# Kernel tuning notes

Measured on AMD Instinct MI355X. Metric: run time of the kernel, lower is better.

The kernel has to match this reference:

```python
import jax, jax.numpy as jnp
import numpy as np

A, B, S, AD, H, NH = 8, 32768, 128, 16, 64, 4
D = H // NH  # attend_dim = 16
MAX_ACTION = 1.0


def setup_inputs() -> dict:
    key = jax.random.key(0)
    ks = jax.random.split(key, 16)
    sc = 0.05
    return {
        'states': jax.random.normal(ks[0], (A, B, S), jnp.float32),
        'actions': jax.random.normal(ks[1], (A, B, AD), jnp.float32),
        'Ws': jax.random.normal(ks[2], (S, H), jnp.float32) * sc,
        'bs': jnp.zeros((H,), jnp.float32),
        'We': jax.random.normal(ks[3], (S + AD, H), jnp.float32) * sc,
        'be': jnp.zeros((H,), jnp.float32),
        'Wk': jax.random.normal(ks[4], (NH, H, D), jnp.float32) * sc,
        'Wsel': jax.random.normal(ks[5], (NH, H, D), jnp.float32) * sc,
        'Wv': jax.random.normal(ks[6], (NH, H, D), jnp.float32) * sc,
        'bv': jnp.zeros((NH, D), jnp.float32),
        'W1': jax.random.normal(ks[7], (2 * H, H), jnp.float32) * sc,
        'b1': jnp.zeros((H,), jnp.float32),
        'W2': jax.random.normal(ks[8], (H, 1), jnp.float32) * sc,
        'b2': jnp.zeros((1,), jnp.float32),
    }


def reference(states, actions, Ws, bs, We, be, Wk, Wsel, Wv, bv, W1, b1, W2, b2):
    # per-agent encoders (shared params, as in the torch module)
    s_enc = jax.nn.relu(jnp.einsum('abs,sh->abh', states, Ws) + bs)          # [A,B,H]
    sa = jnp.concatenate([states, actions / MAX_ACTION], axis=-1)            # [A,B,S+AD]
    sa_enc = jax.nn.relu(jnp.einsum('abi,ih->abh', sa, We) + be)             # [A,B,H]

    # per-head keys / values / selectors (n = head axis)
    keys = jnp.einsum('abh,nhd->nabd', sa_enc, Wk)                           # [NH,A,B,D]
    vals = jax.nn.relu(jnp.einsum('abh,nhd->nabd', sa_enc, Wv) + bv[:, None, None, :])
    sel = jnp.einsum('abh,nhd->nabd', s_enc, Wsel)                           # [NH,A,B,D]

    # exclude-self attention over agents == masked softmax over agent axis j
    logits = jnp.einsum('nibd,njbd->nibj', sel, keys) / jnp.sqrt(jnp.float32(D))
    self_mask = jnp.eye(A, dtype=bool)                                       # [A(i),A(j)]
    logits = jnp.where(self_mask[None, :, None, :], -1e9, logits)
    w = jax.nn.softmax(logits, axis=-1)                                      # [NH,A,B,A]
    other = jnp.einsum('nibj,njbd->nibd', w, vals)                           # [NH,A,B,D]
    other_cat = jnp.transpose(other, (1, 2, 0, 3)).reshape(A, B, NH * D)     # [A,B,H]

    critic_in = jnp.concatenate([sa_enc, other_cat], axis=-1)                # [A,B,2H]
    h = jax.nn.relu(jnp.einsum('abi,ih->abh', critic_in, W1) + b1)
    q = jnp.einsum('abh,ho->abo', h, W2) + b2                                # [A,B,1]
    return q
```

## Files before the change

### kernel.cpp

```cpp
#include <hip/hip_runtime.h>
#include <hip/hip_bf16.h>

#define A_N 8
#define B_N 32768
#define S_N 128
#define AD_N 16

typedef __attribute__((ext_vector_type(8))) short short8;
typedef __attribute__((ext_vector_type(4))) float floatx4;

#define MFMA16(a, b, c) __builtin_amdgcn_mfma_f32_16x16x32_bf16(a, b, c, 0, 0, 0)

__device__ __forceinline__ short f2bf(float f) {
    __hip_bfloat16 h = __float2bfloat16(f);
    return *reinterpret_cast<short*>(&h);
}
__device__ __forceinline__ float bf2f(short s) {
    return __uint_as_float(((unsigned)(unsigned short)s) << 16);
}
__device__ __forceinline__ void pk2(short8& r, int i, float a, float b) {
    __hip_bfloat162 p = __float22bfloat162_rn(make_float2(a, b));
    short2 s = *reinterpret_cast<short2*>(&p);
    r[i] = s.x; r[i + 1] = s.y;
}
__device__ __forceinline__ short8 cvt8(float4 x0, float4 x1) {
    short8 r;
    pk2(r, 0, x0.x, x0.y); pk2(r, 2, x0.z, x0.w);
    pk2(r, 4, x1.x, x1.y); pk2(r, 6, x1.z, x1.w);
    return r;
}
__device__ __forceinline__ void wait_lgkm() {
    asm volatile("s_waitcnt lgkmcnt(0)" ::: "memory");
}

#define OFF_Ws 10752
#define OFF_Wk 19456
#define OFF_Wsel 24064
#define OFF_Wv 28672
#define OFF_W1 33280
#define W_TOTAL 41984

__global__ void prep_weights(const float* __restrict__ Ws, const float* __restrict__ We,
                             const float* __restrict__ Wk, const float* __restrict__ Wsel,
                             const float* __restrict__ Wv, const float* __restrict__ W1,
                             short* __restrict__ w) {
    int idx = blockIdx.x * 256 + threadIdx.x;
    if (idx >= W_TOTAL) return;
    float v;
    if (idx < OFF_Ws)        { int n = idx / 168, k = idx % 168; v = (k < 144) ? We[k * 64 + n] : 0.f; }
    else if (idx < OFF_Wk)   { int i = idx - OFF_Ws;  int n = i / 136, k = i % 136; v = (k < 128) ? Ws[k * 64 + n] : 0.f; }
    else if (idx < OFF_Wsel) { int i = idx - OFF_Wk;  int n = i / 72,  k = i % 72;  v = (k < 64) ? Wk[(n >> 4) * 1024 + k * 16 + (n & 15)] : 0.f; }
    else if (idx < OFF_Wv)   { int i = idx - OFF_Wsel;int n = i / 72,  k = i % 72;  v = (k < 64) ? Wsel[(n >> 4) * 1024 + k * 16 + (n & 15)] : 0.f; }
    else if (idx < OFF_W1)   { int i = idx - OFF_Wv;  int n = i / 72,  k = i % 72;  v = (k < 64) ? Wv[(n >> 4) * 1024 + k * 16 + (n & 15)] : 0.f; }
    else                     { int i = idx - OFF_W1;  int n = i / 136, k = i % 136; v = (k < 128) ? W1[k * 64 + n] : 0.f; }
    w[idx] = f2bf(v);
}

#define ST 72
#define OFF_Eb 41984
#define OFF_Tb 51200
#define OFF_Kb 60416
#define OFF_Vb 69632
#define SMEM_TOT 78848

#define TILES 4

__global__ __launch_bounds__(512, 2)
void attention_critic_mfma(
    const float* __restrict__ states, const float* __restrict__ actions,
    const float* __restrict__ bs, const float* __restrict__ be,
    const float* __restrict__ bv, const float* __restrict__ b1,
    const float* __restrict__ W2, const float* __restrict__ b2,
    const short* __restrict__ wts, float* __restrict__ out)
{
    __shared__ __align__(16) short smem[SMEM_TOT];
    short* lWe   = smem;
    short* lWs   = smem + OFF_Ws;
    short* lWk   = smem + OFF_Wk;
    short* lWsel = smem + OFF_Wsel;
    short* lWv   = smem + OFF_Wv;
    short* lW1   = smem + OFF_W1;
    short* Eb    = smem + OFF_Eb;
    short* Tb    = smem + OFF_Tb;
    short* Kb    = smem + OFF_Kb;
    short* Vb    = smem + OFF_Vb;

    const int tid  = threadIdx.x;
    const int wv   = tid >> 6;
    const int lane = tid & 63;
    const int lq   = lane >> 4;
    const int ln   = lane & 15;
    const int rA   = wv * 16 + ln;
    const int bbase = blockIdx.x * (TILES * 16);

    for (int c = wv; c < 82; c += 8) {
        const unsigned int* g = reinterpret_cast<const unsigned int*>(wts + c * 512) + lane * 4;
        __builtin_amdgcn_global_load_lds(g, reinterpret_cast<unsigned int*>(smem + c * 512), 16, 0, 0);
    }

    const int aA  = ln & 7;
    const int blA = ln >> 3;
    const float* srow = states  + ((long)aA * B_N + bbase + wv * 2 + blA) * S_N;
    const float* arow = actions + ((long)aA * B_N + bbase + wv * 2 + blA) * AD_N;

    float4 ps[8]; float4 pa[2];
    #pragma unroll
    for (int s = 0; s < 4; ++s) {
        ps[2 * s]     = *reinterpret_cast<const float4*>(srow + s * 32 + lq * 8);
        ps[2 * s + 1] = *reinterpret_cast<const float4*>(srow + s * 32 + lq * 8 + 4);
    }
    if (lq < 2) {
        pa[0] = *reinterpret_cast<const float4*>(arow + lq * 8);
        pa[1] = *reinterpret_cast<const float4*>(arow + lq * 8 + 4);
    }
    __syncthreads();

    const floatx4 z = {0.f, 0.f, 0.f, 0.f};

    #pragma unroll 1
    for (int t = 0; t < TILES; ++t) {
        const int b0 = bbase + t * 16;

        floatx4 accE[4] = {z, z, z, z};
        floatx4 accS[4] = {z, z, z, z};
        #pragma unroll
        for (int s = 0; s < 4; ++s) {
            const int kk = s * 32 + lq * 8;
            short8 af = cvt8(ps[2 * s], ps[2 * s + 1]);
            #pragma unroll
            for (int nt = 0; nt < 4; ++nt) {
                short8 bE = *reinterpret_cast<const short8*>(lWe + (nt * 16 + ln) * 168 + kk);
                short8 bS = *reinterpret_cast<const short8*>(lWs + (nt * 16 + ln) * 136 + kk);
                accE[nt] = MFMA16(af, bE, accE[nt]);
                accS[nt] = MFMA16(af, bS, accS[nt]);
            }
        }
        {
            const int kk = 128 + lq * 8;
            short8 af = {0, 0, 0, 0, 0, 0, 0, 0};
            if (lq < 2) af = cvt8(pa[0], pa[1]);
            #pragma unroll
            for (int nt = 0; nt < 4; ++nt) {
                short8 bE = *reinterpret_cast<const short8*>(lWe + (nt * 16 + ln) * 168 + kk);
                accE[nt] = MFMA16(af, bE, accE[nt]);
            }
        }

        if (t + 1 < TILES) {
            srow += 16 * S_N; arow += 16 * AD_N;
            #pragma unroll
            for (int s = 0; s < 4; ++s) {
                ps[2 * s]     = *reinterpret_cast<const float4*>(srow + s * 32 + lq * 8);
                ps[2 * s + 1] = *reinterpret_cast<const float4*>(srow + s * 32 + lq * 8 + 4);
            }
            if (lq < 2) {
                pa[0] = *reinterpret_cast<const float4*>(arow + lq * 8);
                pa[1] = *reinterpret_cast<const float4*>(arow + lq * 8 + 4);
            }
        }

        #pragma unroll
        for (int nt = 0; nt < 4; ++nt) {
            const int col = nt * 16 + ln;
            const float bE = be[col], bS = bs[col];
            #pragma unroll
            for (int i = 0; i < 4; ++i) {
                const int row = wv * 16 + lq * 4 + i;
                Eb[row * ST + col] = f2bf(fmaxf(accE[nt][i] + bE, 0.f));
                Tb[row * ST + col] = f2bf(fmaxf(accS[nt][i] + bS, 0.f));
            }
        }
        wait_lgkm();

        floatx4 accSel[4] = {z, z, z, z};
        #pragma unroll
        for (int s = 0; s < 2; ++s) {
            short8 af = *reinterpret_cast<const short8*>(Tb + rA * ST + s * 32 + lq * 8);
            #pragma unroll
            for (int nt = 0; nt < 4; ++nt)
                accSel[nt] = MFMA16(af, *reinterpret_cast<const short8*>(lWsel + (nt * 16 + ln) * 72 + s * 32 + lq * 8), accSel[nt]);
        }
        #pragma unroll
        for (int nt = 0; nt < 4; ++nt)
            #pragma unroll
            for (int i = 0; i < 4; ++i)
                Tb[(wv * 16 + lq * 4 + i) * ST + nt * 16 + ln] = f2bf(accSel[nt][i]);

        floatx4 accK[4] = {z, z, z, z}, accV[4] = {z, z, z, z};
        #pragma unroll
        for (int s = 0; s < 2; ++s) {
            short8 af = *reinterpret_cast<const short8*>(Eb + rA * ST + s * 32 + lq * 8);
            #pragma unroll
            for (int nt = 0; nt < 4; ++nt) {
                accK[nt] = MFMA16(af, *reinterpret_cast<const short8*>(lWk + (nt * 16 + ln) * 72 + s * 32 + lq * 8), accK[nt]);
                accV[nt] = MFMA16(af, *reinterpret_cast<const short8*>(lWv + (nt * 16 + ln) * 72 + s * 32 + lq * 8), accV[nt]);
            }
        }
        #pragma unroll
        for (int nt = 0; nt < 4; ++nt) {
            const int col = nt * 16 + ln;
            const float bV = bv[col];
            #pragma unroll
            for (int i = 0; i < 4; ++i) {
                const int row = wv * 16 + lq * 4 + i;
                Kb[row * ST + col] = f2bf(accK[nt][i]);
                Vb[row * ST + col] = f2bf(fmaxf(accV[nt][i] + bV, 0.f));
            }
        }
        wait_lgkm();

        {
            const int r3 = lane >> 2;
            const int hn = lane & 3;
            const int a3 = r3 & 7;
            const int rowbase = wv * 16 + (r3 & 8);
            const int co = hn * 16;
            float selv[16];
            short8 s0 = *reinterpret_cast<const short8*>(Tb + (wv * 16 + r3) * ST + co);
            short8 s1 = *reinterpret_cast<const short8*>(Tb + (wv * 16 + r3) * ST + co + 8);
            #pragma unroll
            for (int d = 0; d < 8; ++d) { selv[d] = bf2f(s0[d]); selv[d + 8] = bf2f(s1[d]); }
            float lg[8];
            #pragma unroll
            for (int j = 0; j < 8; ++j) {
                const int rj = rowbase + j;
                short8 k0 = *reinterpret_cast<const short8*>(Kb + rj * ST + co);
                short8 k1 = *reinterpret_cast<const short8*>(Kb + rj * ST + co + 8);
                float acc = 0.f;
                #pragma unroll
                for (int d = 0; d < 8; ++d) acc += selv[d] * bf2f(k0[d]) + selv[d + 8] * bf2f(k1[d]);
                lg[j] = (j == a3) ? -1e9f : acc * 0.25f;
            }
            float m = lg[0];
            #pragma unroll
            for (int j = 1; j < 8; ++j) m = fmaxf(m, lg[j]);
            float e[8], ssum = 0.f;
            #pragma unroll
            for (int j = 0; j < 8; ++j) { e[j] = __expf(lg[j] - m); ssum += e[j]; }
            const float inv = 1.f / ssum;
            float oth[16];
            #pragma unroll
            for (int d = 0; d < 16; ++d) oth[d] = 0.f;
            #pragma unroll
            for (int j = 0; j < 8; ++j) {
                const float wj = e[j] * inv;
                const int rj = rowbase + j;
                short8 v0 = *reinterpret_cast<const short8*>(Vb + rj * ST + co);
                short8 v1 = *reinterpret_cast<const short8*>(Vb + rj * ST + co + 8);
                #pragma unroll
                for (int d = 0; d < 8; ++d) { oth[d] += wj * bf2f(v0[d]); oth[d + 8] += wj * bf2f(v1[d]); }
            }
            short8 o0, o1;
            #pragma unroll
            for (int d = 0; d < 8; ++d) { o0[d] = f2bf(oth[d]); o1[d] = f2bf(oth[d + 8]); }
            *reinterpret_cast<short8*>(Tb + (wv * 16 + r3) * ST + co)     = o0;
            *reinterpret_cast<short8*>(Tb + (wv * 16 + r3) * ST + co + 8) = o1;
        }
        wait_lgkm();

        floatx4 accH[4] = {z, z, z, z};
        #pragma unroll
        for (int s = 0; s < 4; ++s) {
            short8 af = (s < 2)
                ? *reinterpret_cast<const short8*>(Eb + rA * ST + s * 32 + lq * 8)
                : *reinterpret_cast<const short8*>(Tb + rA * ST + (s - 2) * 32 + lq * 8);
            #pragma unroll
            for (int nt = 0; nt < 4; ++nt)
                accH[nt] = MFMA16(af, *reinterpret_cast<const short8*>(lW1 + (nt * 16 + ln) * 136 + s * 32 + lq * 8), accH[nt]);
        }
        float p0 = 0.f, p1 = 0.f, p2 = 0.f, p3 = 0.f;
        #pragma unroll
        for (int nt = 0; nt < 4; ++nt) {
            const int col = nt * 16 + ln;
            const float w2v = W2[col], bb = b1[col];
            p0 += fmaxf(accH[nt][0] + bb, 0.f) * w2v;
            p1 += fmaxf(accH[nt][1] + bb, 0.f) * w2v;
            p2 += fmaxf(accH[nt][2] + bb, 0.f) * w2v;
            p3 += fmaxf(accH[nt][3] + bb, 0.f) * w2v;
        }
        #pragma unroll
        for (int mk = 1; mk < 16; mk <<= 1) {
            p0 += __shfl_xor(p0, mk, 64);
            p1 += __shfl_xor(p1, mk, 64);
            p2 += __shfl_xor(p2, mk, 64);
            p3 += __shfl_xor(p3, mk, 64);
        }
        if (ln == 0) {
            const float b2v = b2[0];
            float pr[4] = {p0, p1, p2, p3};
            #pragma unroll
            for (int i = 0; i < 4; ++i) {
                const int m = lq * 4 + i;
                out[(long)(m & 7) * B_N + b0 + wv * 2 + (m >> 3)] = pr[i] + b2v;
            }
        }
    }
}

extern "C" void kernel_launch(void* const* d_in, const int* in_sizes, int n_in,
                              void* d_out, int out_size, void* d_ws, size_t ws_size,
                              hipStream_t stream) {
    const float* states  = (const float*)d_in[0];
    const float* actions = (const float*)d_in[1];
    const float* Ws      = (const float*)d_in[2];
    const float* bs      = (const float*)d_in[3];
    const float* We      = (const float*)d_in[4];
    const float* be      = (const float*)d_in[5];
    const float* Wk      = (const float*)d_in[6];
    const float* Wsel    = (const float*)d_in[7];
    const float* Wv      = (const float*)d_in[8];
    const float* bv      = (const float*)d_in[9];
    const float* W1      = (const float*)d_in[10];
    const float* b1      = (const float*)d_in[11];
    const float* W2      = (const float*)d_in[12];
    const float* b2      = (const float*)d_in[13];
    short* wts = (short*)d_ws;
    float* out = (float*)d_out;

    prep_weights<<<(W_TOTAL + 255) / 256, 256, 0, stream>>>(Ws, We, Wk, Wsel, Wv, W1, wts);
    attention_critic_mfma<<<B_N / (TILES * 16), 512, 0, stream>>>(
        states, actions, bs, be, bv, b1, W2, b2, wts, out);
}
```

Measured before the change: 257.2 us.

## Keep intermediates in registers via transposed MFMA chaining and MFMA-based attention

Removes all shared-memory staging of activations. Each matmul's output fragment is chained directly as the next MFMA operand, using a channel permutation baked into the weights and transposed operand order. The per-agent attention logits and weighted sum now run as small MFMAs with shuffle-based softmax. Biases are folded into the encoder GEMM through a constant-one input column. Block size grows to 1024 threads with only weights in LDS, which trades register pressure and wasted zero-padded MFMA lanes for removing LDS traffic and barriers.

```diff
diff --git a/kernel.cpp b/kernel.cpp
--- a/kernel.cpp
+++ b/kernel.cpp
@@ -8,6 +8,7 @@
 
 typedef __attribute__((ext_vector_type(8))) short short8;
 typedef __attribute__((ext_vector_type(4))) float floatx4;
+typedef __attribute__((ext_vector_type(4))) int intx4;
 
 #define MFMA16(a, b, c) __builtin_amdgcn_mfma_f32_16x16x32_bf16(a, b, c, 0, 0, 0)
 
@@ -15,8 +16,13 @@
     __hip_bfloat16 h = __float2bfloat16(f);
     return *reinterpret_cast<short*>(&h);
 }
-__device__ __forceinline__ float bf2f(short s) {
-    return __uint_as_float(((unsigned)(unsigned short)s) << 16);
+__device__ __forceinline__ int pk(float a, float b) {
+    __hip_bfloat162 p = __float22bfloat162_rn(make_float2(a, b));
+    return *reinterpret_cast<int*>(&p);
+}
+__device__ __forceinline__ short8 mk8(int a, int b, int c, int d) {
+    intx4 v = {a, b, c, d};
+    return *reinterpret_cast<short8*>(&v);
 }
 __device__ __forceinline__ void pk2(short8& r, int i, float a, float b) {
     __hip_bfloat162 p = __float22bfloat162_rn(make_float2(a, b));
@@ -29,75 +35,86 @@
     pk2(r, 4, x1.x, x1.y); pk2(r, 6, x1.z, x1.w);
     return r;
 }
-__device__ __forceinline__ void wait_lgkm() {
-    asm volatile("s_waitcnt lgkmcnt(0)" ::: "memory");
-}
-
-#define OFF_Ws 10752
-#define OFF_Wk 19456
-#define OFF_Wsel 24064
-#define OFF_Wv 28672
-#define OFF_W1 33280
-#define W_TOTAL 41984
-
-__global__ void prep_weights(const float* __restrict__ Ws, const float* __restrict__ We,
+
+__device__ __forceinline__ int chperm(int p) {
+    return 32 * (p >> 5) + 16 * ((p & 7) >> 2) + 4 * ((p >> 3) & 3) + (p & 3);
+}
+
+#define OFF_Ws   10752
+#define OFF_Wk   21504
+#define OFF_Wsel 26112
+#define OFF_Wv   30720
+#define OFF_W1   35328
+#define W_TOTAL  44032
+
+__global__ void prep_weights(const float* __restrict__ Ws, const float* __restrict__ bs,
+                             const float* __restrict__ We, const float* __restrict__ be,
                              const float* __restrict__ Wk, const float* __restrict__ Wsel,
                              const float* __restrict__ Wv, const float* __restrict__ W1,
                              short* __restrict__ w) {
     int idx = blockIdx.x * 256 + threadIdx.x;
     if (idx >= W_TOTAL) return;
-    float v;
-    if (idx < OFF_Ws)        { int n = idx / 168, k = idx % 168; v = (k < 144) ? We[k * 64 + n] : 0.f; }
-    else if (idx < OFF_Wk)   { int i = idx - OFF_Ws;  int n = i / 136, k = i % 136; v = (k < 128) ? Ws[k * 64 + n] : 0.f; }
-    else if (idx < OFF_Wsel) { int i = idx - OFF_Wk;  int n = i / 72,  k = i % 72;  v = (k < 64) ? Wk[(n >> 4) * 1024 + k * 16 + (n & 15)] : 0.f; }
-    else if (idx < OFF_Wv)   { int i = idx - OFF_Wsel;int n = i / 72,  k = i % 72;  v = (k < 64) ? Wsel[(n >> 4) * 1024 + k * 16 + (n & 15)] : 0.f; }
-    else if (idx < OFF_W1)   { int i = idx - OFF_Wv;  int n = i / 72,  k = i % 72;  v = (k < 64) ? Wv[(n >> 4) * 1024 + k * 16 + (n & 15)] : 0.f; }
-    else                     { int i = idx - OFF_W1;  int n = i / 136, k = i % 136; v = (k < 128) ? W1[k * 64 + n] : 0.f; }
+    float v = 0.f;
+    if (idx < OFF_Ws) {
+        int n = idx / 168, p = idx % 168;
+        v = (p < 144) ? We[p * 64 + n] : (p == 144 ? be[n] : 0.f);
+    } else if (idx < OFF_Wk) {
+        int i = idx - OFF_Ws; int n = i / 168, p = i % 168;
+        v = (p < 128) ? Ws[p * 64 + n] : (p == 144 ? bs[n] : 0.f);
+    } else if (idx < OFF_Wsel) {
+        int i = idx - OFF_Wk; int n = i / 72, p = i % 72;
+        if (p < 64) v = Wk[(n >> 4) * 1024 + chperm(p) * 16 + (n & 15)];
+    } else if (idx < OFF_Wv) {
+        int i = idx - OFF_Wsel; int n = i / 72, p = i % 72;
+        if (p < 64) v = Wsel[(n >> 4) * 1024 + chperm(p) * 16 + (n & 15)];
+    } else if (idx < OFF_W1) {
+        int i = idx - OFF_Wv; int n = i / 72, p = i % 72;
+        if (p < 64) v = Wv[(n >> 4) * 1024 + chperm(p) * 16 + (n & 15)];
+    } else {
+        int i = idx - OFF_W1; int n = i / 136, p = i % 136;
+        if (p < 128) v = W1[chperm(p) * 64 + n];
+    }
     w[idx] = f2bf(v);
 }
 
-#define ST 72
-#define OFF_Eb 41984
-#define OFF_Tb 51200
-#define OFF_Kb 60416
-#define OFF_Vb 69632
-#define SMEM_TOT 78848
-
 #define TILES 4
 
-__global__ __launch_bounds__(512, 2)
+__global__ __launch_bounds__(1024, 4)
 void attention_critic_mfma(
     const float* __restrict__ states, const float* __restrict__ actions,
-    const float* __restrict__ bs, const float* __restrict__ be,
     const float* __restrict__ bv, const float* __restrict__ b1,
     const float* __restrict__ W2, const float* __restrict__ b2,
     const short* __restrict__ wts, float* __restrict__ out)
 {
-    __shared__ __align__(16) short smem[SMEM_TOT];
-    short* lWe   = smem;
-    short* lWs   = smem + OFF_Ws;
-    short* lWk   = smem + OFF_Wk;
-    short* lWsel = smem + OFF_Wsel;
-    short* lWv   = smem + OFF_Wv;
-    short* lW1   = smem + OFF_W1;
-    short* Eb    = smem + OFF_Eb;
-    short* Tb    = smem + OFF_Tb;
-    short* Kb    = smem + OFF_Kb;
-    short* Vb    = smem + OFF_Vb;
+    __shared__ __align__(16) short smem[W_TOTAL];
+    const short* lWe   = smem;
+    const short* lWs   = smem + OFF_Ws;
+    const short* lWk   = smem + OFF_Wk;
+    const short* lWsel = smem + OFF_Wsel;
+    const short* lWv   = smem + OFF_Wv;
+    const short* lW1   = smem + OFF_W1;
 
     const int tid  = threadIdx.x;
     const int wv   = tid >> 6;
     const int lane = tid & 63;
     const int lq   = lane >> 4;
     const int ln   = lane & 15;
-    const int rA   = wv * 16 + ln;
-    const int bbase = blockIdx.x * (TILES * 16);
-
-    for (int c = wv; c < 82; c += 8) {
+
+    for (int c = wv; c < 86; c += 16) {
         const unsigned int* g = reinterpret_cast<const unsigned int*>(wts + c * 512) + lane * 4;
         __builtin_amdgcn_global_load_lds(g, reinterpret_cast<unsigned int*>(smem + c * 512), 16, 0, 0);
     }
 
+    float bv4[4], b14[4], w24[4];
+    #pragma unroll
+    for (int nt = 0; nt < 4; ++nt) {
+        bv4[nt] = bv[nt * 16 + ln];
+        b14[nt] = b1[nt * 16 + ln];
+        w24[nt] = W2[nt * 16 + ln];
+    }
+    const float b2v = b2[0];
+
+    const int bbase = blockIdx.x * (TILES * 32);
     const int aA  = ln & 7;
     const int blA = ln >> 3;
     const float* srow = states  + ((long)aA * B_N + bbase + wv * 2 + blA) * S_N;
@@ -115,39 +132,97 @@
     }
     __syncthreads();
 
-    const floatx4 z = {0.f, 0.f, 0.f, 0.f};
+    const floatx4 z  = {0.f, 0.f, 0.f, 0.f};
+    const short8  z8 = {0, 0, 0, 0, 0, 0, 0, 0};
 
     #pragma unroll 1
     for (int t = 0; t < TILES; ++t) {
-        const int b0 = bbase + t * 16;
-
-        floatx4 accE[4] = {z, z, z, z};
-        floatx4 accS[4] = {z, z, z, z};
-        #pragma unroll
-        for (int s = 0; s < 4; ++s) {
+        const int b0 = bbase + t * 32;
+
+        short8 xf[5];
+        #pragma unroll
+        for (int s = 0; s < 4; ++s) xf[s] = cvt8(ps[2 * s], ps[2 * s + 1]);
+        {
+            short8 xt = z8;
+            if (lq < 2) xt = cvt8(pa[0], pa[1]);
+            else if (lq == 2) xt[0] = (short)0x3F80;
+            xf[4] = xt;
+        }
+        floatx4 accE[4] = {z, z, z, z}, accS[4] = {z, z, z, z};
+        #pragma unroll
+        for (int s = 0; s < 5; ++s) {
             const int kk = s * 32 + lq * 8;
-            short8 af = cvt8(ps[2 * s], ps[2 * s + 1]);
             #pragma unroll
             for (int nt = 0; nt < 4; ++nt) {
-                short8 bE = *reinterpret_cast<const short8*>(lWe + (nt * 16 + ln) * 168 + kk);
-                short8 bS = *reinterpret_cast<const short8*>(lWs + (nt * 16 + ln) * 136 + kk);
-                accE[nt] = MFMA16(af, bE, accE[nt]);
-                accS[nt] = MFMA16(af, bS, accS[nt]);
-            }
-        }
-        {
-            const int kk = 128 + lq * 8;
-            short8 af = {0, 0, 0, 0, 0, 0, 0, 0};
-            if (lq < 2) af = cvt8(pa[0], pa[1]);
+                accE[nt] = MFMA16(*reinterpret_cast<const short8*>(lWe + (nt * 16 + ln) * 168 + kk), xf[s], accE[nt]);
+                accS[nt] = MFMA16(*reinterpret_cast<const short8*>(lWs + (nt * 16 + ln) * 168 + kk), xf[s], accS[nt]);
+            }
+        }
+        int pE[4][2], pS[4][2];
+        #pragma unroll
+        for (int nt = 0; nt < 4; ++nt) {
+            pE[nt][0] = pk(fmaxf(accE[nt][0], 0.f), fmaxf(accE[nt][1], 0.f));
+            pE[nt][1] = pk(fmaxf(accE[nt][2], 0.f), fmaxf(accE[nt][3], 0.f));
+            pS[nt][0] = pk(fmaxf(accS[nt][0], 0.f), fmaxf(accS[nt][1], 0.f));
+            pS[nt][1] = pk(fmaxf(accS[nt][2], 0.f), fmaxf(accS[nt][3], 0.f));
+        }
+        short8 fE[2] = { mk8(pE[0][0], pE[0][1], pE[1][0], pE[1][1]),
+                         mk8(pE[2][0], pE[2][1], pE[3][0], pE[3][1]) };
+        short8 fS[2] = { mk8(pS[0][0], pS[0][1], pS[1][0], pS[1][1]),
+                         mk8(pS[2][0], pS[2][1], pS[3][0], pS[3][1]) };
+
+        floatx4 accK[4] = {z, z, z, z}, accSl[4] = {z, z, z, z};
+        floatx4 accV[4] = {z, z, z, z}, accH[4] = {z, z, z, z};
+        #pragma unroll
+        for (int s = 0; s < 2; ++s) {
+            const int kk = s * 32 + lq * 8;
             #pragma unroll
             for (int nt = 0; nt < 4; ++nt) {
-                short8 bE = *reinterpret_cast<const short8*>(lWe + (nt * 16 + ln) * 168 + kk);
-                accE[nt] = MFMA16(af, bE, accE[nt]);
-            }
+                const int rw = (nt * 16 + ln);
+                accK[nt]  = MFMA16(*reinterpret_cast<const short8*>(lWk   + rw * 72 + kk), fE[s], accK[nt]);
+                accSl[nt] = MFMA16(*reinterpret_cast<const short8*>(lWsel + rw * 72 + kk), fS[s], accSl[nt]);
+                accV[nt]  = MFMA16(fE[s], *reinterpret_cast<const short8*>(lWv + rw * 72  + kk), accV[nt]);
+                accH[nt]  = MFMA16(fE[s], *reinterpret_cast<const short8*>(lW1 + rw * 136 + kk), accH[nt]);
+            }
+        }
+        int pV[4][2];
+        #pragma unroll
+        for (int nt = 0; nt < 4; ++nt) {
+            pV[nt][0] = pk(fmaxf(accV[nt][0] + bv4[nt], 0.f), fmaxf(accV[nt][1] + bv4[nt], 0.f));
+            pV[nt][1] = pk(fmaxf(accV[nt][2] + bv4[nt], 0.f), fmaxf(accV[nt][3] + bv4[nt], 0.f));
+        }
+
+        int pO[4][2];
+        const bool sameb = ((lq >> 1) == (ln >> 3));
+        #pragma unroll
+        for (int nt = 0; nt < 4; ++nt) {
+            short8 fa = mk8(pk(accK[nt][0],  accK[nt][1]),  pk(accK[nt][2],  accK[nt][3]),  0, 0);
+            short8 fb = mk8(pk(accSl[nt][0], accSl[nt][1]), pk(accSl[nt][2], accSl[nt][3]), 0, 0);
+            floatx4 L = MFMA16(fa, fb, z);
+            float lg[4];
+            #pragma unroll
+            for (int i = 0; i < 4; ++i) {
+                const bool valid = sameb && (4 * lq + i != ln);
+                lg[i] = valid ? L[i] * 0.25f : -1e9f;
+            }
+            float m = fmaxf(fmaxf(lg[0], lg[1]), fmaxf(lg[2], lg[3]));
+            m = fmaxf(m, __shfl_xor(m, 16, 64));
+            m = fmaxf(m, __shfl_xor(m, 32, 64));
+            float e0 = __expf(lg[0] - m), e1 = __expf(lg[1] - m);
+            float e2 = __expf(lg[2] - m), e3 = __expf(lg[3] - m);
+            float ss = e0 + e1 + e2 + e3;
+            ss += __shfl_xor(ss, 16, 64);
+            ss += __shfl_xor(ss, 32, 64);
+            const float inv = 1.f / ss;
+            short8 fp = mk8(pk(e0 * inv, e1 * inv), pk(e2 * inv, e3 * inv), 0, 0);
+            short8 fv = mk8(pV[nt][0], pV[nt][1], 0, 0);
+            floatx4 O = MFMA16(fv, fp, z);
+            pO[nt][0] = pk(O[0], O[1]);
+            pO[nt][1] = pk(O[2], O[3]);
         }
 
         if (t + 1 < TILES) {
-            srow += 16 * S_N; arow += 16 * AD_N;
+            srow += 32 * S_N; arow += 32 * AD_N;
             #pragma unroll
             for (int s = 0; s < 4; ++s) {
                 ps[2 * s]     = *reinterpret_cast<const float4*>(srow + s * 32 + lq * 8);
@@ -159,124 +234,22 @@
             }
         }
 
-        #pragma unroll
-        for (int nt = 0; nt < 4; ++nt) {
-            const int col = nt * 16 + ln;
-            const float bE = be[col], bS = bs[col];
-            #pragma unroll
-            for (int i = 0; i < 4; ++i) {
-                const int row = wv * 16 + lq * 4 + i;
-                Eb[row * ST + col] = f2bf(fmaxf(accE[nt][i] + bE, 0.f));
-                Tb[row * ST + col] = f2bf(fmaxf(accS[nt][i] + bS, 0.f));
-            }
-        }
-        wait_lgkm();
-
-        floatx4 accSel[4] = {z, z, z, z};
-        #pragma unroll
-        for (int s = 0; s < 2; ++s) {
-            short8 af = *reinterpret_cast<const short8*>(Tb + rA * ST + s * 32 + lq * 8);
+        short8 fO[2] = { mk8(pO[0][0], pO[0][1], pO[1][0], pO[1][1]),
+                         mk8(pO[2][0], pO[2][1], pO[3][0], pO[3][1]) };
+        #pragma unroll
+        for (int s = 2; s < 4; ++s) {
+            const int kk = s * 32 + lq * 8;
             #pragma unroll
             for (int nt = 0; nt < 4; ++nt)
-                accSel[nt] = MFMA16(af, *reinterpret_cast<const short8*>(lWsel + (nt * 16 + ln) * 72 + s * 32 + lq * 8), accSel[nt]);
-        }
-        #pragma unroll
-        for (int nt = 0; nt < 4; ++nt)
-            #pragma unroll
-            for (int i = 0; i < 4; ++i)
-                Tb[(wv * 16 + lq * 4 + i) * ST + nt * 16 + ln] = f2bf(accSel[nt][i]);
-
-        floatx4 accK[4] = {z, z, z, z}, accV[4] = {z, z, z, z};
-        #pragma unroll
-        for (int s = 0; s < 2; ++s) {
-            short8 af = *reinterpret_cast<const short8*>(Eb + rA * ST + s * 32 + lq * 8);
-            #pragma unroll
-            for (int nt = 0; nt < 4; ++nt) {
-                accK[nt] = MFMA16(af, *reinterpret_cast<const short8*>(lWk + (nt * 16 + ln) * 72 + s * 32 + lq * 8), accK[nt]);
-                accV[nt] = MFMA16(af, *reinterpret_cast<const short8*>(lWv + (nt * 16 + ln) * 72 + s * 32 + lq * 8), accV[nt]);
-            }
-        }
-        #pragma unroll
-        for (int nt = 0; nt < 4; ++nt) {
-            const int col = nt * 16 + ln;
-            const float bV = bv[col];
-            #pragma unroll
-            for (int i = 0; i < 4; ++i) {
-                const int row = wv * 16 + lq * 4 + i;
-                Kb[row * ST + col] = f2bf(accK[nt][i]);
-                Vb[row * ST + col] = f2bf(fmaxf(accV[nt][i] + bV, 0.f));
-            }
-        }
-        wait_lgkm();
-
-        {
-            const int r3 = lane >> 2;
-            const int hn = lane & 3;
-            const int a3 = r3 & 7;
-            const int rowbase = wv * 16 + (r3 & 8);
-            const int co = hn * 16;
-            float selv[16];
-            short8 s0 = *reinterpret_cast<const short8*>(Tb + (wv * 16 + r3) * ST + co);
-            short8 s1 = *reinterpret_cast<const short8*>(Tb + (wv * 16 + r3) * ST + co + 8);
-            #pragma unroll
-            for (int d = 0; d < 8; ++d) { selv[d] = bf2f(s0[d]); selv[d + 8] = bf2f(s1[d]); }
-            float lg[8];
-            #pragma unroll
-            for (int j = 0; j < 8; ++j) {
-                const int rj = rowbase + j;
-                short8 k0 = *reinterpret_cast<const short8*>(Kb + rj * ST + co);
-                short8 k1 = *reinterpret_cast<const short8*>(Kb + rj * ST + co + 8);
-                float acc = 0.f;
-                #pragma unroll
-                for (int d = 0; d < 8; ++d) acc += selv[d] * bf2f(k0[d]) + selv[d + 8] * bf2f(k1[d]);
-                lg[j] = (j == a3) ? -1e9f : acc * 0.25f;
-            }
-            float m = lg[0];
-            #pragma unroll
-            for (int j = 1; j < 8; ++j) m = fmaxf(m, lg[j]);
-            float e[8], ssum = 0.f;
-            #pragma unroll
-            for (int j = 0; j < 8; ++j) { e[j] = __expf(lg[j] - m); ssum += e[j]; }
-            const float inv = 1.f / ssum;
-            float oth[16];
-            #pragma unroll
-            for (int d = 0; d < 16; ++d) oth[d] = 0.f;
-            #pragma unroll
-            for (int j = 0; j < 8; ++j) {
-                const float wj = e[j] * inv;
-                const int rj = rowbase + j;
-                short8 v0 = *reinterpret_cast<const short8*>(Vb + rj * ST + co);
-                short8 v1 = *reinterpret_cast<const short8*>(Vb + rj * ST + co + 8);
-                #pragma unroll
-                for (int d = 0; d < 8; ++d) { oth[d] += wj * bf2f(v0[d]); oth[d + 8] += wj * bf2f(v1[d]); }
-            }
-            short8 o0, o1;
-            #pragma unroll
-            for (int d = 0; d < 8; ++d) { o0[d] = f2bf(oth[d]); o1[d] = f2bf(oth[d + 8]); }
-            *reinterpret_cast<short8*>(Tb + (wv * 16 + r3) * ST + co)     = o0;
-            *reinterpret_cast<short8*>(Tb + (wv * 16 + r3) * ST + co + 8) = o1;
-        }
-        wait_lgkm();
-
-        floatx4 accH[4] = {z, z, z, z};
-        #pragma unroll
-        for (int s = 0; s < 4; ++s) {
-            short8 af = (s < 2)
-                ? *reinterpret_cast<const short8*>(Eb + rA * ST + s * 32 + lq * 8)
-                : *reinterpret_cast<const short8*>(Tb + rA * ST + (s - 2) * 32 + lq * 8);
-            #pragma unroll
-            for (int nt = 0; nt < 4; ++nt)
-                accH[nt] = MFMA16(af, *reinterpret_cast<const short8*>(lW1 + (nt * 16 + ln) * 136 + s * 32 + lq * 8), accH[nt]);
+                accH[nt] = MFMA16(fO[s - 2], *reinterpret_cast<const short8*>(lW1 + (nt * 16 + ln) * 136 + kk), accH[nt]);
         }
         float p0 = 0.f, p1 = 0.f, p2 = 0.f, p3 = 0.f;
         #pragma unroll
         for (int nt = 0; nt < 4; ++nt) {
-            const int col = nt * 16 + ln;
-            const float w2v = W2[col], bb = b1[col];
-            p0 += fmaxf(accH[nt][0] + bb, 0.f) * w2v;
-            p1 += fmaxf(accH[nt][1] + bb, 0.f) * w2v;
-            p2 += fmaxf(accH[nt][2] + bb, 0.f) * w2v;
-            p3 += fmaxf(accH[nt][3] + bb, 0.f) * w2v;
+            p0 += fmaxf(accH[nt][0] + b14[nt], 0.f) * w24[nt];
+            p1 += fmaxf(accH[nt][1] + b14[nt], 0.f) * w24[nt];
+            p2 += fmaxf(accH[nt][2] + b14[nt], 0.f) * w24[nt];
+            p3 += fmaxf(accH[nt][3] + b14[nt], 0.f) * w24[nt];
         }
         #pragma unroll
         for (int mk = 1; mk < 16; mk <<= 1) {
@@ -286,12 +259,11 @@
             p3 += __shfl_xor(p3, mk, 64);
         }
         if (ln == 0) {
-            const float b2v = b2[0];
             float pr[4] = {p0, p1, p2, p3};
             #pragma unroll
             for (int i = 0; i < 4; ++i) {
-                const int m = lq * 4 + i;
-                out[(long)(m & 7) * B_N + b0 + wv * 2 + (m >> 3)] = pr[i] + b2v;
+                const int slot = lq * 4 + i;
+                out[(long)(slot & 7) * B_N + b0 + wv * 2 + (slot >> 3)] = pr[i] + b2v;
             }
         }
     }
@@ -317,7 +289,7 @@
     short* wts = (short*)d_ws;
     float* out = (float*)d_out;
 
-    prep_weights<<<(W_TOTAL + 255) / 256, 256, 0, stream>>>(Ws, We, Wk, Wsel, Wv, W1, wts);
-    attention_critic_mfma<<<B_N / (TILES * 16), 512, 0, stream>>>(
-        states, actions, bs, be, bv, b1, W2, b2, wts, out);
-}
+    prep_weights<<<(W_TOTAL + 255) / 256, 256, 0, stream>>>(Ws, bs, We, be, Wk, Wsel, Wv, W1, wts);
+    attention_critic_mfma<<<B_N / (TILES * 32), 1024, 0, stream>>>(
+        states, actions, bv, b1, W2, b2, wts, out);
+}
```

New measurement: 615.0 us. 2.39x slower.
